# Kernel tuning notes

Measured on AMD Instinct MI355X. Metric: run time of the kernel, lower is better.

Reference implementation:

```python
import jax, jax.numpy as jnp
import numpy as np

HID = 512


def _lstm_params(key, in_dim, hid):
    k = 1.0 / np.sqrt(hid)
    ks = jax.random.split(key, 4)
    W_ih = jax.random.uniform(ks[0], (4 * hid, in_dim), minval=-k, maxval=k)
    W_hh = jax.random.uniform(ks[1], (4 * hid, hid), minval=-k, maxval=k)
    b_ih = jax.random.uniform(ks[2], (4 * hid,), minval=-k, maxval=k)
    b_hh = jax.random.uniform(ks[3], (4 * hid,), minval=-k, maxval=k)
    return W_ih, W_hh, b_ih, b_hh


def _linear_params(key, in_dim, out_dim):
    k = 1.0 / np.sqrt(in_dim)
    k1, k2 = jax.random.split(key)
    W = jax.random.uniform(k1, (out_dim, in_dim), minval=-k, maxval=k)
    b = jax.random.uniform(k2, (out_dim,), minval=-k, maxval=k)
    return W, b


def setup_inputs() -> dict:
    key = jax.random.key(0)
    ks = jax.random.split(key, 8)
    state_action = jax.random.normal(ks[0], (32768, 19), dtype=jnp.float32)
    W_ih1, W_hh1, b_ih1, b_hh1 = _lstm_params(ks[1], 19, HID)
    W_ih2, W_hh2, b_ih2, b_hh2 = _lstm_params(ks[2], 19, HID)
    W_xyz, b_xyz = _linear_params(ks[3], HID, 3)
    W_zeta, b_zeta = _linear_params(ks[4], HID, 3)
    W_uvw, b_uvw = _linear_params(ks[5], HID, 3)
    W_pqr, b_pqr = _linear_params(ks[6], HID, 3)
    return dict(state_action=state_action,
                W_ih1=W_ih1, W_hh1=W_hh1, b_ih1=b_ih1, b_hh1=b_hh1,
                W_ih2=W_ih2, W_hh2=W_hh2, b_ih2=b_ih2, b_hh2=b_hh2,
                W_xyz=W_xyz, b_xyz=b_xyz, W_zeta=W_zeta, b_zeta=b_zeta,
                W_uvw=W_uvw, b_uvw=b_uvw, W_pqr=W_pqr, b_pqr=b_pqr)


def _lstm_step(gates_x, h, c, W_hh, b_hh, hid):
    # torch LSTMCell gate order: input, forget, cell(g), output
    g = gates_x + h @ W_hh.T + b_hh
    i = jax.nn.sigmoid(g[:hid])
    f = jax.nn.sigmoid(g[hid:2 * hid])
    gg = jnp.tanh(g[2 * hid:3 * hid])
    o = jax.nn.sigmoid(g[3 * hid:])
    c_new = f * c + i * gg
    h_new = o * jnp.tanh(c_new)
    return h_new, c_new


def reference(state_action, W_ih1, W_hh1, b_ih1, b_hh1,
              W_ih2, W_hh2, b_ih2, b_hh2,
              W_xyz, b_xyz, W_zeta, b_zeta, W_uvw, b_uvw, W_pqr, b_pqr):
    hid = W_hh1.shape[1]
    # precompute input projections for all timesteps (one big GEMM each)
    gx1 = state_action @ W_ih1.T + b_ih1  # [H, 4*hid]
    gx2 = state_action @ W_ih2.T + b_ih2  # [H, 4*hid]

    def step(carry, gx):
        h1, c1, h2, c2 = carry
        g1, g2 = gx
        h1, c1 = _lstm_step(g1, h1, c1, W_hh1, b_hh1, hid)
        h2, c2 = _lstm_step(g2, h2, c2, W_hh2, b_hh2, hid)
        return (h1, c1, h2, c2), (h1, h2)

    z = jnp.zeros((hid,), dtype=state_action.dtype)
    _, (h1s, h2s) = jax.lax.scan(step, (z, z, z, z), (gx1, gx2))
    xyz = h1s @ W_xyz.T + b_xyz
    zeta = h2s @ W_zeta.T + b_zeta
    uvw = h1s @ W_uvw.T + b_uvw
    pqr = h2s @ W_pqr.T + b_pqr
    # original returns a list of [1,12] tensors; we return the stacked [H,12]
    return jnp.concatenate([xyz, zeta, uvw, pqr], axis=1)
```

## Files before the change

### kernel.cpp

```cpp
#include <hip/hip_runtime.h>

#define T_STEPS 32768
#define THREADS 256
#define NLAUNCH 256
#define D_SLOTS 4

typedef unsigned int uint32;
typedef unsigned long long ull;
typedef unsigned int u32x4 __attribute__((ext_vector_type(4)));


__device__ inline float fsig(float x) {
    return __builtin_amdgcn_rcpf(1.f + __expf(-x));
}
__device__ inline float ftanh(float x) {
    return 1.f - 2.f * __builtin_amdgcn_rcpf(1.f + __expf(2.f * x));
}
__device__ inline float wred64(float x) {
    x += __shfl_xor(x, 1);  x += __shfl_xor(x, 2);  x += __shfl_xor(x, 4);
    x += __shfl_xor(x, 8);  x += __shfl_xor(x, 16); x += __shfl_xor(x, 32);
    return x;
}

__device__ inline void poll16(const ull* p, u32x4& v) {
    asm volatile("global_load_dwordx4 %0, %1, off sc0 nt\n\t"
                 "s_waitcnt vmcnt(0)"
                 : "=v"(v) : "v"(p) : "memory");
}

__device__ inline uint32 a_add(uint32* p, uint32 v) {
    return __hip_atomic_fetch_add(p, v, __ATOMIC_RELAXED, __HIP_MEMORY_SCOPE_AGENT);
}
__device__ inline uint32 a_ld(const uint32* p) {
    return __hip_atomic_load(p, __ATOMIC_RELAXED, __HIP_MEMORY_SCOPE_AGENT);
}
__device__ inline void a_st(uint32* p, uint32 v) {
    __hip_atomic_store(p, v, __ATOMIC_RELAXED, __HIP_MEMORY_SCOPE_AGENT);
}
__device__ inline ull rescue_rmw(ull* p) {
    return __hip_atomic_fetch_add(p, 0ull, __ATOMIC_RELAXED, __HIP_MEMORY_SCOPE_AGENT);
}

__global__ __launch_bounds__(THREADS, 1)
void lstm_persistent(const float* __restrict__ sa,
                     const float* __restrict__ W_ih1, const float* __restrict__ W_hh1,
                     const float* __restrict__ b_ih1, const float* __restrict__ b_hh1,
                     const float* __restrict__ W_ih2, const float* __restrict__ W_hh2,
                     const float* __restrict__ b_ih2, const float* __restrict__ b_hh2,
                     const float* __restrict__ W_xyz, const float* __restrict__ b_xyz,
                     const float* __restrict__ W_zeta, const float* __restrict__ b_zeta,
                     const float* __restrict__ W_uvw, const float* __restrict__ b_uvw,
                     const float* __restrict__ W_pqr, const float* __restrict__ b_pqr,
                     float* __restrict__ out, ull* hrot, uint32* claim)
{
    const int tid  = threadIdx.x;
    const int wv   = tid >> 6;
    const int lane = tid & 63;

    __shared__ int s_lstm, s_w;

    if (tid == 0) {
        uint32 xcc;
        asm volatile("s_getreg_b32 %0, hwreg(HW_REG_XCC_ID)" : "=s"(xcc));
        xcc &= 7;
        uint32* cnt     = claim;
        uint32* rankcnt = claim + 8;
        uint32* grank   = claim + 16;

        int lstm = -1, w = 0;
        uint32 slot = a_add(&cnt[xcc], 1);
        if (slot < 32) {
            w = (int)slot;
            if (slot == 31) {
                uint32 rank = a_add(rankcnt, 1);
                a_st(&grank[xcc], (rank < 2) ? (rank + 1) : 0xFEu);
            }
            uint32 g;
            long spins = 0;
            for (;;) {
                g = a_ld(&grank[xcc]);
                if (g != 0) break;
                if (a_ld(rankcnt) >= 2 && ++spins > 200000) { g = 0xFEu; break; }
            }
            if (g != 0xFEu) lstm = (int)g - 1;
        }
        s_lstm = lstm; s_w = w;
    }
    __syncthreads();
    const int lstm = s_lstm;
    const int w    = s_w;
    if (lstm < 0) return;

    const float* W_ih = lstm ? W_ih2 : W_ih1;
    const float* W_hh = lstm ? W_hh2 : W_hh1;
    const float* b_ih = lstm ? b_ih2 : b_ih1;
    const float* b_hh = lstm ? b_hh2 : b_hh1;
    const float* W_a  = lstm ? W_zeta : W_xyz;
    const float* W_b  = lstm ? W_pqr  : W_uvw;

    ull* hb = hrot + (size_t)lstm * D_SLOTS * 512;

    __shared__ __align__(16) float h_lds[2][528];
    __shared__ float sa_lds[2][20];
    __shared__ float wih_lds[64 * 19];
    __shared__ float pj_lds[6 * 512];

    const int r  = lane >> 2;
    const int cb = lane & 3;
    const int gt = r >> 2;
    const int jj = r & 3;
    const int G  = gt * 512 + (w << 4) + (wv << 2) + jj;

    float wa[128];
    {
        const float4* wp4 = (const float4*)(W_hh + (size_t)G * 512 + cb * 128);
        #pragma unroll
        for (int k = 0; k < 32; ++k) {
            float4 t4 = wp4[k];
            asm volatile("v_accvgpr_write_b32 %0, %1" : "=a"(wa[4 * k + 0]) : "v"(t4.x));
            asm volatile("v_accvgpr_write_b32 %0, %1" : "=a"(wa[4 * k + 1]) : "v"(t4.y));
            asm volatile("v_accvgpr_write_b32 %0, %1" : "=a"(wa[4 * k + 2]) : "v"(t4.z));
            asm volatile("v_accvgpr_write_b32 %0, %1" : "=a"(wa[4 * k + 3]) : "v"(t4.w));
        }
    }
    for (int idx = tid; idx < 64 * 19; idx += THREADS) {
        int rr = idx / 19, kk = idx - rr * 19;
        int v2 = rr >> 4, r2 = rr & 15;
        int G2 = (r2 >> 2) * 512 + (w << 4) + (v2 << 2) + (r2 & 3);
        wih_lds[idx] = W_ih[G2 * 19 + kk];
    }
    for (int idx = tid; idx < 6 * 512; idx += THREADS) {
        int o = idx >> 9, c = idx & 511;
        pj_lds[idx] = (o < 3) ? W_a[o * 512 + c] : W_b[(o - 3) * 512 + c];
    }
    const float bsum = b_ih[G] + b_hh[G];

    float ball[16];
    #pragma unroll
    for (int k = 0; k < 16; ++k)
        asm volatile("v_accvgpr_write_b32 %0, %1" : "=a"(ball[k]) : "v"(bsum));

    float pb[6] = {0.f, 0.f, 0.f, 0.f, 0.f, 0.f};
    if (wv == 1) {
        const float* ba = lstm ? b_zeta : b_xyz;
        const float* bb = lstm ? b_pqr  : b_uvw;
        #pragma unroll
        for (int o = 0; o < 3; ++o) { pb[o] = ba[o]; pb[o + 3] = bb[o]; }
    }

    float c_reg = 0.0f;
    int   thr   = 64;
    __syncthreads();

    for (int t = 0; t <= T_STEPS; ++t) {
        const int b = t & 1;

        float sval = 0.f;
        const bool do_sa = (wv == 3 && lane < 19 && t < T_STEPS);
        if (do_sa) sval = sa[(size_t)t * 19 + lane];

        {
            const int j    = 2 * tid;
            const int pidx = ((j >> 7) * 132) + (j & 127);
            if (t > 0) {
                ull* sp = hb + (size_t)((uint32)(t - 1) & (D_SLOTS - 1)) * 512 + j;
                const uint32 tag = (uint32)t;
                u32x4 pv;
                int spin = 0;
                for (;;) {
                    poll16(sp, pv);
                    if (pv.x == tag && pv.z == tag) break;
                    if (++spin >= thr) {
                        ull a = rescue_rmw(sp);
                        ull bq = rescue_rmw(sp + 1);
                        if ((uint32)a == tag && (uint32)bq == tag) {
                            pv.x = (uint32)a; pv.y = (uint32)(a >> 32);
                            pv.z = (uint32)bq; pv.w = (uint32)(bq >> 32);
                            break;
                        }
                        thr = 2;
                        spin = 0;
                    }
                }
                h_lds[b][pidx]     = __uint_as_float(pv.y);
                h_lds[b][pidx + 1] = __uint_as_float(pv.w);
            } else {
                h_lds[b][pidx] = 0.f;
                h_lds[b][pidx + 1] = 0.f;
            }
        }
        if (do_sa) sa_lds[b][lane] = sval;
        __syncthreads();

        if (t > 0 && wv == 1 && (((t - 1) & 31) == w)) {
            float a0 = 0.f, a1 = 0.f, a2 = 0.f, a3 = 0.f, a4 = 0.f, a5 = 0.f;
            #pragma unroll
            for (int m = 0; m < 8; ++m) {
                int c = lane + (m << 6);
                float hv = h_lds[b][((c >> 7) * 132) + (c & 127)];
                a0 = fmaf(hv, pj_lds[c],        a0);
                a1 = fmaf(hv, pj_lds[512 + c],  a1);
                a2 = fmaf(hv, pj_lds[1024 + c], a2);
                a3 = fmaf(hv, pj_lds[1536 + c], a3);
                a4 = fmaf(hv, pj_lds[2048 + c], a4);
                a5 = fmaf(hv, pj_lds[2560 + c], a5);
            }
            a0 = wred64(a0); a1 = wred64(a1); a2 = wred64(a2);
            a3 = wred64(a3); a4 = wred64(a4); a5 = wred64(a5);
            if (lane == 0) {
                size_t ob = (size_t)(t - 1) * 12;
                int ca = 3 * lstm, cbb = 6 + 3 * lstm;
                out[ob + ca + 0]  = a0 + pb[0];
                out[ob + ca + 1]  = a1 + pb[1];
                out[ob + ca + 2]  = a2 + pb[2];
                out[ob + cbb + 0] = a3 + pb[3];
                out[ob + cbb + 1] = a4 + pb[4];
                out[ob + cbb + 2] = a5 + pb[5];
            }
        }
        if (t == T_STEPS) break;

        float part = (cb == 0) ? bsum : 0.f;
        {
            const int base = (wv * 16 + r) * 19;
            const int k0 = cb * 5;
            #pragma unroll
            for (int i = 0; i < 5; ++i) {
                int k = k0 + i;
                if (k < 19) part = fmaf(sa_lds[b][k], wih_lds[base + k], part);
            }
        }
        {
            const float4* hp4 = (const float4*)(&h_lds[b][cb * 132]);
            float ax = 0.f, ay = 0.f, az = 0.f, aw2 = 0.f;
            #pragma unroll
            for (int k = 0; k < 32; ++k) {
                float4 hv = hp4[k];
                float w0, w1, w2, w3;
                asm volatile("v_accvgpr_read_b32 %0, %1" : "=v"(w0) : "a"(wa[4 * k + 0]));
                asm volatile("v_accvgpr_read_b32 %0, %1" : "=v"(w1) : "a"(wa[4 * k + 1]));
                asm volatile("v_accvgpr_read_b32 %0, %1" : "=v"(w2) : "a"(wa[4 * k + 2]));
                asm volatile("v_accvgpr_read_b32 %0, %1" : "=v"(w3) : "a"(wa[4 * k + 3]));
                ax  = fmaf(w0, hv.x, ax);
                ay  = fmaf(w1, hv.y, ay);
                az  = fmaf(w2, hv.z, az);
                aw2 = fmaf(w3, hv.w, aw2);
            }
            part += (ax + ay) + (az + aw2);
        }
        part += __shfl_xor(part, 1);
        part += __shfl_xor(part, 2);

        float act = (gt == 2) ? ftanh(part) : fsig(part);
        float i_v = __shfl(act, 4 * jj);
        float f_v = __shfl(act, 16 + 4 * jj);
        float g_v = __shfl(act, 32 + 4 * jj);
        float o_v = __shfl(act, 48 + 4 * jj);

        if (r < 4 && cb == 0) {
            c_reg = f_v * c_reg + i_v * g_v;
            float hn = o_v * ftanh(c_reg);
            ull pk = ((ull)__float_as_uint(hn) << 32) | (ull)(uint32)(t + 1);
            __hip_atomic_store(
                &hb[(size_t)((uint32)t & (D_SLOTS - 1)) * 512 + (w << 4) + (wv << 2) + r],
                pk, __ATOMIC_RELAXED, __HIP_MEMORY_SCOPE_WORKGROUP);
        }
    }

    if (lstm < -1) {
        float s = 0.f;
        #pragma unroll
        for (int k = 0; k < 16; ++k) {
            float tv;
            asm volatile("v_accvgpr_read_b32 %0, %1" : "=v"(tv) : "a"(ball[k]));
            s += tv;
        }
        ((float*)claim)[31] = s;
    }
}

extern "C" void kernel_launch(void* const* d_in, const int* in_sizes, int n_in,
                              void* d_out, int out_size, void* d_ws, size_t ws_size,
                              hipStream_t stream)
{
    const float* sa    = (const float*)d_in[0];
    const float* W_ih1 = (const float*)d_in[1];
    const float* W_hh1 = (const float*)d_in[2];
    const float* b_ih1 = (const float*)d_in[3];
    const float* b_hh1 = (const float*)d_in[4];
    const float* W_ih2 = (const float*)d_in[5];
    const float* W_hh2 = (const float*)d_in[6];
    const float* b_ih2 = (const float*)d_in[7];
    const float* b_hh2 = (const float*)d_in[8];
    const float* W_xyz = (const float*)d_in[9];
    const float* b_xyz = (const float*)d_in[10];
    const float* W_zeta= (const float*)d_in[11];
    const float* b_zeta= (const float*)d_in[12];
    const float* W_uvw = (const float*)d_in[13];
    const float* b_uvw = (const float*)d_in[14];
    const float* W_pqr = (const float*)d_in[15];
    const float* b_pqr = (const float*)d_in[16];

    float*  out   = (float*)d_out;
    ull*    hrot  = (ull*)d_ws;
    uint32* claim = (uint32*)((char*)d_ws + 2 * D_SLOTS * 512 * sizeof(ull));

    hipMemsetAsync(d_ws, 0, 2 * D_SLOTS * 512 * sizeof(ull) + 128, stream);

    lstm_persistent<<<NLAUNCH, THREADS, 0, stream>>>(
        sa, W_ih1, W_hh1, b_ih1, b_hh1, W_ih2, W_hh2, b_ih2, b_hh2,
        W_xyz, b_xyz, W_zeta, b_zeta, W_uvw, b_uvw, W_pqr, b_pqr,
        out, hrot, claim);
}
```

Measured before the change: 77.58 ms.

## Make each wavefront poll full hidden state independently, removing per-step block barrier

Each wavefront now polls all 512 hidden values itself with four vector loads into a private LDS slice. It also broadcasts the state-action inputs via shuffles instead of shared memory, which removes the per-timestep __syncthreads between the four waves. The output projection runs after the gate computation, so it no longer delays publishing h. This removes block-level synchronization from the critical recurrence path. The cost is four times more global polling traffic per block and more rescue atomics.

After: 70.48 ms. 1.1x faster.

```diff
diff --git a/kernel.cpp b/kernel.cpp
--- a/kernel.cpp
+++ b/kernel.cpp
@@ -22,10 +22,14 @@
     return x;
 }
 
-__device__ inline void poll16(const ull* p, u32x4& v) {
-    asm volatile("global_load_dwordx4 %0, %1, off sc0 nt\n\t"
+__device__ inline void poll4x(const ull* p, u32x4& v0, u32x4& v1, u32x4& v2, u32x4& v3) {
+    asm volatile("global_load_dwordx4 %0, %4, off sc0 nt\n\t"
+                 "global_load_dwordx4 %1, %4, off offset:1024 sc0 nt\n\t"
+                 "global_load_dwordx4 %2, %4, off offset:2048 sc0 nt\n\t"
+                 "global_load_dwordx4 %3, %4, off offset:3072 sc0 nt\n\t"
                  "s_waitcnt vmcnt(0)"
-                 : "=v"(v) : "v"(p) : "memory");
+                 : "=&v"(v0), "=&v"(v1), "=&v"(v2), "=&v"(v3)
+                 : "v"(p) : "memory");
 }
 
 __device__ inline uint32 a_add(uint32* p, uint32 v) {
@@ -100,10 +104,10 @@
 
     ull* hb = hrot + (size_t)lstm * D_SLOTS * 512;
 
-    __shared__ __align__(16) float h_lds[2][528];
-    __shared__ float sa_lds[2][20];
+    __shared__ __align__(16) float hw_all[4][528];
     __shared__ float wih_lds[64 * 19];
     __shared__ float pj_lds[6 * 512];
+    float* hw = hw_all[wv];
 
     const int r  = lane >> 2;
     const int cb = lane & 3;
@@ -152,52 +156,107 @@
     int   thr   = 64;
     __syncthreads();
 
+    const bool projector = (wv == 1);
+
     for (int t = 0; t <= T_STEPS; ++t) {
-        const int b = t & 1;
-
-        float sval = 0.f;
-        const bool do_sa = (wv == 3 && lane < 19 && t < T_STEPS);
-        if (do_sa) sval = sa[(size_t)t * 19 + lane];
-
-        {
-            const int j    = 2 * tid;
-            const int pidx = ((j >> 7) * 132) + (j & 127);
-            if (t > 0) {
-                ull* sp = hb + (size_t)((uint32)(t - 1) & (D_SLOTS - 1)) * 512 + j;
-                const uint32 tag = (uint32)t;
-                u32x4 pv;
-                int spin = 0;
-                for (;;) {
-                    poll16(sp, pv);
-                    if (pv.x == tag && pv.z == tag) break;
-                    if (++spin >= thr) {
-                        ull a = rescue_rmw(sp);
-                        ull bq = rescue_rmw(sp + 1);
-                        if ((uint32)a == tag && (uint32)bq == tag) {
-                            pv.x = (uint32)a; pv.y = (uint32)(a >> 32);
-                            pv.z = (uint32)bq; pv.w = (uint32)(bq >> 32);
-                            break;
-                        }
-                        thr = 2;
-                        spin = 0;
+        if (t == T_STEPS && !(projector && w == ((T_STEPS - 1) & 31))) break;
+
+        float sav = 0.f;
+        if (lane < 19 && t < T_STEPS) sav = sa[(size_t)t * 19 + lane];
+
+        if (t > 0) {
+            ull* sp = hb + (size_t)((uint32)(t - 1) & (D_SLOTS - 1)) * 512 + 2 * lane;
+            const uint32 tag = (uint32)t;
+            u32x4 v0, v1, v2, v3;
+            int spin = 0;
+            for (;;) {
+                poll4x(sp, v0, v1, v2, v3);
+                if (v0.x == tag && v0.z == tag && v1.x == tag && v1.z == tag &&
+                    v2.x == tag && v2.z == tag && v3.x == tag && v3.z == tag) break;
+                if (++spin >= thr) {
+                    ull a0 = rescue_rmw(sp),       a1 = rescue_rmw(sp + 1);
+                    ull b0 = rescue_rmw(sp + 128), b1 = rescue_rmw(sp + 129);
+                    ull c0 = rescue_rmw(sp + 256), c1 = rescue_rmw(sp + 257);
+                    ull d0 = rescue_rmw(sp + 384), d1 = rescue_rmw(sp + 385);
+                    if ((uint32)a0 == tag && (uint32)a1 == tag &&
+                        (uint32)b0 == tag && (uint32)b1 == tag &&
+                        (uint32)c0 == tag && (uint32)c1 == tag &&
+                        (uint32)d0 == tag && (uint32)d1 == tag) {
+                        v0.y = (uint32)(a0 >> 32); v0.w = (uint32)(a1 >> 32);
+                        v1.y = (uint32)(b0 >> 32); v1.w = (uint32)(b1 >> 32);
+                        v2.y = (uint32)(c0 >> 32); v2.w = (uint32)(c1 >> 32);
+                        v3.y = (uint32)(d0 >> 32); v3.w = (uint32)(d1 >> 32);
+                        break;
                     }
+                    thr = 2;
+                    spin = 0;
                 }
-                h_lds[b][pidx]     = __uint_as_float(pv.y);
-                h_lds[b][pidx + 1] = __uint_as_float(pv.w);
-            } else {
-                h_lds[b][pidx] = 0.f;
-                h_lds[b][pidx + 1] = 0.f;
-            }
-        }
-        if (do_sa) sa_lds[b][lane] = sval;
-        __syncthreads();
-
-        if (t > 0 && wv == 1 && (((t - 1) & 31) == w)) {
+            }
+            *(float2*)&hw[      2 * lane] = make_float2(__uint_as_float(v0.y), __uint_as_float(v0.w));
+            *(float2*)&hw[132 + 2 * lane] = make_float2(__uint_as_float(v1.y), __uint_as_float(v1.w));
+            *(float2*)&hw[264 + 2 * lane] = make_float2(__uint_as_float(v2.y), __uint_as_float(v2.w));
+            *(float2*)&hw[396 + 2 * lane] = make_float2(__uint_as_float(v3.y), __uint_as_float(v3.w));
+        } else if (t == 0) {
+            *(float2*)&hw[      2 * lane] = make_float2(0.f, 0.f);
+            *(float2*)&hw[132 + 2 * lane] = make_float2(0.f, 0.f);
+            *(float2*)&hw[264 + 2 * lane] = make_float2(0.f, 0.f);
+            *(float2*)&hw[396 + 2 * lane] = make_float2(0.f, 0.f);
+        }
+
+        if (t < T_STEPS) {
+            float part = (cb == 0) ? bsum : 0.f;
+            {
+                const int base = (wv * 16 + r) * 19;
+                const int k0 = cb * 5;
+                #pragma unroll
+                for (int i = 0; i < 5; ++i) {
+                    int k = k0 + i;
+                    if (k < 19) part = fmaf(__shfl(sav, k), wih_lds[base + k], part);
+                }
+            }
+            {
+                const float4* hp4 = (const float4*)&hw[cb * 132];
+                float ax = 0.f, ay = 0.f, az = 0.f, aw2 = 0.f;
+                #pragma unroll
+                for (int k = 0; k < 32; ++k) {
+                    float4 hv = hp4[k];
+                    float w0, w1, w2, w3;
+                    asm volatile("v_accvgpr_read_b32 %0, %1" : "=v"(w0) : "a"(wa[4 * k + 0]));
+                    asm volatile("v_accvgpr_read_b32 %0, %1" : "=v"(w1) : "a"(wa[4 * k + 1]));
+                    asm volatile("v_accvgpr_read_b32 %0, %1" : "=v"(w2) : "a"(wa[4 * k + 2]));
+                    asm volatile("v_accvgpr_read_b32 %0, %1" : "=v"(w3) : "a"(wa[4 * k + 3]));
+                    ax  = fmaf(w0, hv.x, ax);
+                    ay  = fmaf(w1, hv.y, ay);
+                    az  = fmaf(w2, hv.z, az);
+                    aw2 = fmaf(w3, hv.w, aw2);
+                }
+                part += (ax + ay) + (az + aw2);
+            }
+            part += __shfl_xor(part, 1);
+            part += __shfl_xor(part, 2);
+
+            float act = (gt == 2) ? ftanh(part) : fsig(part);
+            float i_v = __shfl(act, 4 * jj);
+            float f_v = __shfl(act, 16 + 4 * jj);
+            float g_v = __shfl(act, 32 + 4 * jj);
+            float o_v = __shfl(act, 48 + 4 * jj);
+
+            if (r < 4 && cb == 0) {
+                c_reg = f_v * c_reg + i_v * g_v;
+                float hn = o_v * ftanh(c_reg);
+                ull pk = ((ull)__float_as_uint(hn) << 32) | (ull)(uint32)(t + 1);
+                __hip_atomic_store(
+                    &hb[(size_t)((uint32)t & (D_SLOTS - 1)) * 512 + (w << 4) + (wv << 2) + r],
+                    pk, __ATOMIC_RELAXED, __HIP_MEMORY_SCOPE_WORKGROUP);
+            }
+        }
+
+        if (t > 0 && projector && (((t - 1) & 31) == w)) {
             float a0 = 0.f, a1 = 0.f, a2 = 0.f, a3 = 0.f, a4 = 0.f, a5 = 0.f;
             #pragma unroll
             for (int m = 0; m < 8; ++m) {
                 int c = lane + (m << 6);
-                float hv = h_lds[b][((c >> 7) * 132) + (c & 127)];
+                float hv = hw[((c >> 7) * 132) + (c & 127)];
                 a0 = fmaf(hv, pj_lds[c],        a0);
                 a1 = fmaf(hv, pj_lds[512 + c],  a1);
                 a2 = fmaf(hv, pj_lds[1024 + c], a2);
@@ -217,53 +276,6 @@
                 out[ob + cbb + 1] = a4 + pb[4];
                 out[ob + cbb + 2] = a5 + pb[5];
             }
-        }
-        if (t == T_STEPS) break;
-
-        float part = (cb == 0) ? bsum : 0.f;
-        {
-            const int base = (wv * 16 + r) * 19;
-            const int k0 = cb * 5;
-            #pragma unroll
-            for (int i = 0; i < 5; ++i) {
-                int k = k0 + i;
-                if (k < 19) part = fmaf(sa_lds[b][k], wih_lds[base + k], part);
-            }
-        }
-        {
-            const float4* hp4 = (const float4*)(&h_lds[b][cb * 132]);
-            float ax = 0.f, ay = 0.f, az = 0.f, aw2 = 0.f;
-            #pragma unroll
-            for (int k = 0; k < 32; ++k) {
-                float4 hv = hp4[k];
-                float w0, w1, w2, w3;
-                asm volatile("v_accvgpr_read_b32 %0, %1" : "=v"(w0) : "a"(wa[4 * k + 0]));
-                asm volatile("v_accvgpr_read_b32 %0, %1" : "=v"(w1) : "a"(wa[4 * k + 1]));
-                asm volatile("v_accvgpr_read_b32 %0, %1" : "=v"(w2) : "a"(wa[4 * k + 2]));
-                asm volatile("v_accvgpr_read_b32 %0, %1" : "=v"(w3) : "a"(wa[4 * k + 3]));
-                ax  = fmaf(w0, hv.x, ax);
-                ay  = fmaf(w1, hv.y, ay);
-                az  = fmaf(w2, hv.z, az);
-                aw2 = fmaf(w3, hv.w, aw2);
-            }
-            part += (ax + ay) + (az + aw2);
-        }
-        part += __shfl_xor(part, 1);
-        part += __shfl_xor(part, 2);
-
-        float act = (gt == 2) ? ftanh(part) : fsig(part);
-        float i_v = __shfl(act, 4 * jj);
-        float f_v = __shfl(act, 16 + 4 * jj);
-        float g_v = __shfl(act, 32 + 4 * jj);
-        float o_v = __shfl(act, 48 + 4 * jj);
-
-        if (r < 4 && cb == 0) {
-            c_reg = f_v * c_reg + i_v * g_v;
-            float hn = o_v * ftanh(c_reg);
-            ull pk = ((ull)__float_as_uint(hn) << 32) | (ull)(uint32)(t + 1);
-            __hip_atomic_store(
-                &hb[(size_t)((uint32)t & (D_SLOTS - 1)) * 512 + (w << 4) + (wv << 2) + r],
-                pk, __ATOMIC_RELAXED, __HIP_MEMORY_SCOPE_WORKGROUP);
         }
     }
 
```
